# Optimization experiments

Hardware: AMD Instinct MI355X
Metric: run time of the kernel (lower is better)

## Reference

```python
import jax, jax.numpy as jnp
import numpy as np

B, S, D = 1, 2048, 4096          # batch, seqlen, model dim
H, KVH, HD = 32, 8, 128          # query heads, kv heads, head dim
W = 1024                         # sliding window
ROPE_THETA = 10000.0


def _rope(t, cos, sin):
    # t: [b, s, h, hd]; complex pairing matches torch.view_as_complex on reshape(..., hd//2, 2)
    a = t[..., 0::2]
    b = t[..., 1::2]
    out_r = a * cos - b * sin
    out_i = a * sin + b * cos
    return jnp.stack([out_r, out_i], axis=-1).reshape(t.shape)


def setup_inputs() -> dict:
    key = jax.random.key(0)
    ks = jax.random.split(key, 5)
    x = jax.random.normal(ks[0], (1, B, S, D), dtype=jnp.float32)
    wq = jax.random.normal(ks[1], (H * HD, D), dtype=jnp.float32) * 0.02
    wk = jax.random.normal(ks[2], (KVH * HD, D), dtype=jnp.float32) * 0.02
    wv = jax.random.normal(ks[3], (KVH * HD, D), dtype=jnp.float32) * 0.02
    wo = jax.random.normal(ks[4], (D, H * HD), dtype=jnp.float32) * 0.02
    # rotary frequencies: freqs_cis[s, hd/2] = exp(i * s * theta^{-2k/hd})
    inv_freq = 1.0 / (ROPE_THETA ** (jnp.arange(0, HD, 2, dtype=jnp.float32) / HD))
    angles = jnp.arange(S, dtype=jnp.float32)[:, None] * inv_freq[None, :]  # [S, HD/2]
    freqs_cos = jnp.cos(angles)
    freqs_sin = jnp.sin(angles)
    # sliding-window causal mask (additive)
    i = jnp.arange(S)
    allowed = (i[:, None] >= i[None, :]) & (i[:, None] - i[None, :] < W)
    mask = jnp.where(allowed, 0.0, -1e9).astype(jnp.float32)
    positions = jnp.arange(S, dtype=jnp.int64)
    return {"x": x, "wq": wq, "wk": wk, "wv": wv, "wo": wo,
            "freqs_cos": freqs_cos, "freqs_sin": freqs_sin,
            "mask": mask, "positions": positions}


def reference(x, wq, wk, wv, wo, freqs_cos, freqs_sin, mask, positions):
    xs = x[0]                                   # [B, S, D]
    xq = (xs @ wq.T).reshape(B, S, H, HD)
    xk = (xs @ wk.T).reshape(B, S, KVH, HD)
    xv = (xs @ wv.T).reshape(B, S, KVH, HD)
    cos = freqs_cos[None, :, None, :]           # [1, S, 1, HD/2]
    sin = freqs_sin[None, :, None, :]
    xq = _rope(xq, cos, sin)
    xk = _rope(xk, cos, sin)
    # GQA: repeat_interleave kv heads to match query heads (prefill path)
    rep = H // KVH
    k = jnp.repeat(xk, rep, axis=2)             # [B, S, H, HD]
    v = jnp.repeat(xv, rep, axis=2)
    scale = HD ** -0.5
    scores = jnp.einsum('bqhd,bkhd->bhqk', xq, k) * scale + mask[None, None]
    probs = jax.nn.softmax(scores, axis=-1)
    out = jnp.einsum('bhqk,bkhd->bqhd', probs, v).reshape(B, S, H * HD)
    return (out @ wo.T)[None]                   # [1, B, S, D]
```

## Files before the change

### kernel.cpp

```cpp
#include <hip/hip_runtime.h>
#include <hip/hip_bf16.h>


typedef __attribute__((ext_vector_type(8))) short short8;
typedef __attribute__((ext_vector_type(4))) float floatx4;
typedef unsigned short u16;
typedef unsigned int u32;

__device__ __forceinline__ u16 f2bf(float f) {
  u32 u = __builtin_bit_cast(u32, f);
  u32 r = u + 0x7FFFu + ((u >> 16) & 1u);
  return (u16)(r >> 16);
}

#define GLDS16(g, l)                                                     \
  __builtin_amdgcn_global_load_lds(                                      \
      (const __attribute__((address_space(1))) u32*)(g),                 \
      (__attribute__((address_space(3))) u32*)(l), 16, 0, 0)

#define SB() __builtin_amdgcn_sched_barrier(0)

__global__ __launch_bounds__(256) void cast_all(
    const float* __restrict__ x, const float* __restrict__ wq,
    const float* __restrict__ wk, const float* __restrict__ wv,
    const float* __restrict__ wo, u16* __restrict__ xb, u16* __restrict__ wqb,
    u16* __restrict__ wkb, u16* __restrict__ wvb, u16* __restrict__ wob) {
  const int tid = blockIdx.x * blockDim.x + threadIdx.x;
  const int stride = gridDim.x * blockDim.x;
  auto seg = [&](const float* __restrict__ in, u16* __restrict__ out, int n4) {
    for (int i = tid; i < n4; i += stride) {
      float4 v = ((const float4*)in)[i];
      ushort4 o;
      o.x = f2bf(v.x); o.y = f2bf(v.y); o.z = f2bf(v.z); o.w = f2bf(v.w);
      ((ushort4*)out)[i] = o;
    }
  };
  seg(x, xb, 2097152);
  seg(wq, wqb, 4194304);
  seg(wk, wkb, 1048576);
  seg(wv, wvb, 1048576);
  seg(wo, wob, 4194304);
}

template <int IS_QKV>
__global__ __launch_bounds__(512, 2) void gemm_t(
    const u16* __restrict__ A, const u16* __restrict__ B, void* __restrict__ Cq,
    u16* __restrict__ Ck, u16* __restrict__ Cv, const float* __restrict__ fcos,
    const float* __restrict__ fsin) {
  constexpr int BM = IS_QKV ? 256 : 128;
  constexpr int BN = IS_QKV ? 192 : 256;
  constexpr int MFR = BM / 32;
  constexpr int NFR = BN / 64;
  constexpr int WC = BN / 4;
  constexpr int ASZ = BM * 128;
  constexpr int BSZ = BN * 128;
  constexpr int NCA = ASZ / 8192;
  constexpr int NCB = BSZ / 8192;
  __shared__ u16 lds[(2 * ASZ + 3 * BSZ) / 2];
  const int K = 4096;

  int bm, bx;
  if constexpr (IS_QKV) {
    bm = blockIdx.x & 7;
    bx = blockIdx.x >> 3;
  } else {
    const int xcd = blockIdx.x & 7;
    const int j = blockIdx.x >> 3;
    bm = xcd * 2 + (j & 1);
    bx = j >> 1;
  }
  const int m0 = bm * BM, n0 = bx * BN;

  const int t = threadIdx.x, l = t & 63, w = t >> 6;
  const int li = l & 15, g = l >> 4;
  const int wm = w >> 2, wn = w & 3;

  const int srow = t >> 3;
  const int sslot = (t & 7) ^ (srow & 7);
  const u16* gA = A + (size_t)(m0 + srow) * K + sslot * 8;
  const u16* gB = B + (size_t)(n0 + srow) * K + sslot * 8;
  const int dst = t * 16;

  char* A0p = (char*)lds;
  char* A1p = A0p + ASZ;
  char* B0p = A0p + 2 * ASZ;
  char* B1p = B0p + BSZ;
  char* B2p = B1p + BSZ;

  auto stA = [&](char* base, int kt, int c) {
    GLDS16(gA + (size_t)c * 64 * K + kt, base + c * 8192 + dst);
  };
  auto stB = [&](char* base, int kt, int c) {
    GLDS16(gB + (size_t)c * 64 * K + kt, base + c * 8192 + dst);
  };

  int offA[2][MFR], offB[2][NFR];
#pragma unroll
  for (int kh = 0; kh < 2; kh++) {
#pragma unroll
    for (int mf = 0; mf < MFR; mf++) {
      int r = wm * (BM / 2) + mf * 16 + li;
      offA[kh][mf] = r * 128 + ((((kh << 2) | g) ^ (r & 7)) << 4);
    }
#pragma unroll
    for (int nf = 0; nf < NFR; nf++) {
      int r = wn * WC + nf * 16 + li;
      offB[kh][nf] = r * 128 + ((((kh << 2) | g) ^ (r & 7)) << 4);
    }
  }

  floatx4 acc[MFR][NFR] = {};
  const int NT = K / 64;

#pragma unroll
  for (int c = 0; c < NCB; c++) stB(B0p, 0, c);
#pragma unroll
  for (int c = 0; c < NCA; c++) stA(A0p, 0, c);
#pragma unroll
  for (int c = 0; c < NCB; c++) stB(B1p, 64, c);
  if constexpr (IS_QKV) asm volatile("s_waitcnt vmcnt(3)" ::: "memory");
  else                  asm volatile("s_waitcnt vmcnt(4)" ::: "memory");
  __builtin_amdgcn_s_barrier();

  for (int tt = 0; tt < NT; ++tt) {
    SB();
    const char* Ac = A0p;
    const char* Bc = B0p;
    const int kt1 = (tt + 1) * 64, kt2 = (tt + 2) * 64;
    const bool s1 = (tt + 1 < NT), s2 = (tt + 2 < NT);

    if constexpr (IS_QKV) {
      short8 a0[8], b0[3], a1[8], b1[3];
#pragma unroll
      for (int nf = 0; nf < 3; nf++) b0[nf] = *(const short8*)(Bc + offB[0][nf]);
#pragma unroll
      for (int mf = 0; mf < 8; mf++) a0[mf] = *(const short8*)(Ac + offA[0][mf]);
      if (s1) { stA(A1p, kt1, 0); stA(A1p, kt1, 1); stA(A1p, kt1, 2); stA(A1p, kt1, 3); }
#pragma unroll
      for (int mf = 0; mf < 8; mf++)
#pragma unroll
        for (int nf = 0; nf < 3; nf++)
          acc[mf][nf] = __builtin_amdgcn_mfma_f32_16x16x32_bf16(a0[mf], b0[nf], acc[mf][nf], 0, 0, 0);
#pragma unroll
      for (int nf = 0; nf < 3; nf++) b1[nf] = *(const short8*)(Bc + offB[1][nf]);
#pragma unroll
      for (int mf = 0; mf < 8; mf++) a1[mf] = *(const short8*)(Ac + offA[1][mf]);
      if (s2) { stB(B2p, kt2, 0); stB(B2p, kt2, 1); stB(B2p, kt2, 2); }
#pragma unroll
      for (int mf = 0; mf < 8; mf++)
#pragma unroll
        for (int nf = 0; nf < 3; nf++)
          acc[mf][nf] = __builtin_amdgcn_mfma_f32_16x16x32_bf16(a1[mf], b1[nf], acc[mf][nf], 0, 0, 0);
      SB();
      if (s2) asm volatile("s_waitcnt vmcnt(3)" ::: "memory");
      else    asm volatile("s_waitcnt vmcnt(0)" ::: "memory");
      __builtin_amdgcn_s_barrier();
    } else {
      short8 a0[4], b0[4], a1[4], b1[4];
#pragma unroll
      for (int mf = 0; mf < 4; mf++) a0[mf] = *(const short8*)(Ac + offA[0][mf]);
#pragma unroll
      for (int nf = 0; nf < 4; nf++) b0[nf] = *(const short8*)(Bc + offB[0][nf]);
      if (s1) { stA(A1p, kt1, 0); stA(A1p, kt1, 1); }
#pragma unroll
      for (int mf = 0; mf < 4; mf++)
#pragma unroll
        for (int nf = 0; nf < 4; nf++)
          acc[mf][nf] = __builtin_amdgcn_mfma_f32_16x16x32_bf16(a0[mf], b0[nf], acc[mf][nf], 0, 0, 0);
#pragma unroll
      for (int mf = 0; mf < 4; mf++) a1[mf] = *(const short8*)(Ac + offA[1][mf]);
#pragma unroll
      for (int nf = 0; nf < 4; nf++) b1[nf] = *(const short8*)(Bc + offB[1][nf]);
      if (s2) { stB(B2p, kt2, 0); stB(B2p, kt2, 1); stB(B2p, kt2, 2); stB(B2p, kt2, 3); }
#pragma unroll
      for (int mf = 0; mf < 4; mf++)
#pragma unroll
        for (int nf = 0; nf < 4; nf++)
          acc[mf][nf] = __builtin_amdgcn_mfma_f32_16x16x32_bf16(a1[mf], b1[nf], acc[mf][nf], 0, 0, 0);
      SB();
      if (s2) asm volatile("s_waitcnt vmcnt(4)" ::: "memory");
      else    asm volatile("s_waitcnt vmcnt(0)" ::: "memory");
      __builtin_amdgcn_s_barrier();
    }

    char* tmpA = A0p; A0p = A1p; A1p = tmpA;
    char* tmpB = B0p; B0p = B1p; B1p = B2p; B2p = tmpB;
  }

  const float scale = 0.08838834764831845f;
#pragma unroll
  for (int mf = 0; mf < MFR; mf++) {
#pragma unroll
    for (int nf = 0; nf < NFR; nf++) {
      const int row0 = m0 + wm * (BM / 2) + mf * 16 + 4 * g;
      const int c = n0 + wn * WC + nf * 16 + li;
      if constexpr (!IS_QKV) {
        float* Cf = (float*)Cq;
#pragma unroll
        for (int r = 0; r < 4; r++) Cf[(size_t)(row0 + r) * 4096 + c] = acc[mf][nf][r];
      } else {
        if (c < 5120) {
          const int hd = c & 127;
          const int pp = hd >> 1;
          const bool even = (hd & 1) == 0;
#pragma unroll
          for (int r = 0; r < 4; r++) {
            const int row = row0 + r;
            float cv = fcos[row * 64 + pp];
            float sv = fsin[row * 64 + pp];
            float v = acc[mf][nf][r];
            float pv = __shfl_xor(v, 1);
            float o = even ? (v * cv - pv * sv) : (pv * sv + v * cv);
            if (c < 4096) {
              ((u16*)Cq)[(size_t)row * 4096 + c] = f2bf(o * scale);
            } else {
              Ck[(size_t)row * 1024 + (c - 4096)] = f2bf(o);
            }
          }
        } else {
          u32 lo = (u32)f2bf(acc[mf][nf][0]) | ((u32)f2bf(acc[mf][nf][1]) << 16);
          u32 hi = (u32)f2bf(acc[mf][nf][2]) | ((u32)f2bf(acc[mf][nf][3]) << 16);
          uint2 val; val.x = lo; val.y = hi;
          *(uint2*)(&Cv[(size_t)(c - 5120) * 2048 + row0]) = val;
        }
      }
    }
  }
}

__global__ __launch_bounds__(256) void attn_kernel(const u16* __restrict__ Q,
                                                   const u16* __restrict__ K,
                                                   const u16* __restrict__ Vt,
                                                   u16* __restrict__ O) {
  __shared__ u16 Ks[2][64 * 128];
  __shared__ u16 Vs[2][128 * 64];
  __shared__ u16 Ps[4][16 * 72];

  const int t = threadIdx.x, l = t & 63, w = t >> 6;
  const int li = l & 15, g = l >> 4;
  const int q0 = blockIdx.x * 64;
  const int h = blockIdx.y;
  const int kvh = h >> 2;
  const int qw = q0 + w * 16;

  short8 qf[4];
  {
    const u16* qp = Q + (size_t)(qw + li) * 4096 + h * 128 + g * 8;
#pragma unroll
    for (int kk = 0; kk < 4; kk++) qf[kk] = *(const short8*)(qp + kk * 32);
  }

  const u16* gK[4];
  const u16* gV[4];
  int ldsOff[4];
#pragma unroll
  for (int i = 0; i < 4; i++) {
    int rK = 16 * w + 4 * i + (l >> 4);
    int sK = (l & 15) ^ (rK & 7);
    gK[i] = K + (size_t)rK * 1024 + kvh * 128 + sK * 8;
    int rV = 32 * w + 8 * i + (l >> 3);
    int sV = (l & 7) ^ (rV & 7);
    gV[i] = Vt + (size_t)(kvh * 128 + rV) * 2048 + sV * 8;
    ldsOff[i] = (4 * w + i) * 1024;
  }

  int offK[4][4];
#pragma unroll
  for (int n = 0; n < 4; n++) {
    int r = 16 * n + li;
#pragma unroll
    for (int kk = 0; kk < 4; kk++)
      offK[n][kk] = r * 256 + (((kk * 4 + g) ^ (r & 7)) << 4);
  }
  int offV[2][8];
#pragma unroll
  for (int kb = 0; kb < 2; kb++)
#pragma unroll
    for (int dt = 0; dt < 8; dt++) {
      int d = dt * 16 + li;
      offV[kb][dt] = d * 128 + (((kb * 4 + g) ^ (d & 7)) << 4);
    }

  float mrow[4] = {-1e30f, -1e30f, -1e30f, -1e30f};
  float lsum[4] = {0.f, 0.f, 0.f, 0.f};
  floatx4 accO[8] = {};

  int klo = q0 - 1023;
  if (klo < 0) klo = 0;
  klo &= ~63;
  const int nt = (q0 + 64 - klo) >> 6;

  auto stage = [&](int buf, int k0) {
    char* ksb = (char*)&Ks[buf][0];
    char* vsb = (char*)&Vs[buf][0];
#pragma unroll
    for (int i = 0; i < 4; i++) GLDS16(gK[i] + (size_t)k0 * 1024, ksb + ldsOff[i]);
#pragma unroll
    for (int i = 0; i < 4; i++) GLDS16(gV[i] + k0, vsb + ldsOff[i]);
  };

  stage(0, klo);
  asm volatile("s_waitcnt vmcnt(0)" ::: "memory");
  __builtin_amdgcn_s_barrier();

  for (int it = 0; it < nt; it++) {
    const int k0 = klo + (it << 6);
    if (it + 1 < nt) stage((it + 1) & 1, k0 + 64);

    if (k0 <= qw + 15 && k0 + 63 >= qw - 1023) {
      const char* kb = (const char*)&Ks[it & 1][0];
      const char* vb = (const char*)&Vs[it & 1][0];
      floatx4 s[4] = {};
      __builtin_amdgcn_s_setprio(1);
#pragma unroll
      for (int kk = 0; kk < 4; kk++)
#pragma unroll
        for (int n = 0; n < 4; n++) {
          short8 kf = *(const short8*)(kb + offK[n][kk]);
          s[n] = __builtin_amdgcn_mfma_f32_16x16x32_bf16(qf[kk], kf, s[n], 0, 0, 0);
        }
      __builtin_amdgcn_s_setprio(0);
      const bool full = (k0 + 63 <= qw) && (k0 >= qw + 15 - 1023);
      if (!full) {
#pragma unroll
        for (int n = 0; n < 4; n++) {
          const int kc = k0 + n * 16 + li;
#pragma unroll
          for (int r = 0; r < 4; r++) {
            const int qr = qw + 4 * g + r;
            if (kc > qr || qr - kc > 1023) s[n][r] = -__builtin_inff();
          }
        }
      }
      float rm[4];
#pragma unroll
      for (int r = 0; r < 4; r++)
        rm[r] = fmaxf(fmaxf(s[0][r], s[1][r]), fmaxf(s[2][r], s[3][r]));
#pragma unroll
      for (int msk = 1; msk <= 8; msk <<= 1)
#pragma unroll
        for (int r = 0; r < 4; r++) rm[r] = fmaxf(rm[r], __shfl_xor(rm[r], msk));
      float al[4];
#pragma unroll
      for (int r = 0; r < 4; r++) {
        float mn = fmaxf(mrow[r], rm[r]);
        al[r] = __expf(mrow[r] - mn);
        mrow[r] = mn;
        lsum[r] *= al[r];
      }
#pragma unroll
      for (int dt = 0; dt < 8; dt++)
#pragma unroll
        for (int r = 0; r < 4; r++) accO[dt][r] *= al[r];
      float rs[4] = {0.f, 0.f, 0.f, 0.f};
      u16* pw = &Ps[w][0];
#pragma unroll
      for (int n = 0; n < 4; n++)
#pragma unroll
        for (int r = 0; r < 4; r++) {
          float p = __expf(s[n][r] - mrow[r]);
          rs[r] += p;
          pw[(4 * g + r) * 72 + n * 16 + li] = f2bf(p);
        }
#pragma unroll
      for (int msk = 1; msk <= 8; msk <<= 1)
#pragma unroll
        for (int r = 0; r < 4; r++) rs[r] += __shfl_xor(rs[r], msk);
#pragma unroll
      for (int r = 0; r < 4; r++) lsum[r] += rs[r];
      short8 pa[2];
#pragma unroll
      for (int kbi = 0; kbi < 2; kbi++)
        pa[kbi] = *(const short8*)((const char*)&Ps[w][0] + li * 144 + kbi * 64 + g * 16);
      __builtin_amdgcn_s_setprio(1);
#pragma unroll
      for (int kbi = 0; kbi < 2; kbi++)
#pragma unroll
        for (int dt = 0; dt < 8; dt++) {
          short8 vf = *(const short8*)(vb + offV[kbi][dt]);
          accO[dt] = __builtin_amdgcn_mfma_f32_16x16x32_bf16(pa[kbi], vf, accO[dt], 0, 0, 0);
        }
      __builtin_amdgcn_s_setprio(0);
    }
    asm volatile("s_waitcnt vmcnt(0)" ::: "memory");
    __builtin_amdgcn_s_barrier();
  }

  float inv[4];
#pragma unroll
  for (int r = 0; r < 4; r++) inv[r] = 1.0f / lsum[r];
#pragma unroll
  for (int dt = 0; dt < 8; dt++)
#pragma unroll
    for (int r = 0; r < 4; r++)
      O[(size_t)(qw + 4 * g + r) * 4096 + h * 128 + dt * 16 + li] =
          f2bf(accO[dt][r] * inv[r]);
}

extern "C" void kernel_launch(void* const* d_in, const int* in_sizes, int n_in,
                              void* d_out, int out_size, void* d_ws, size_t ws_size,
                              hipStream_t stream) {
  const float* x    = (const float*)d_in[0];
  const float* wq   = (const float*)d_in[1];
  const float* wk   = (const float*)d_in[2];
  const float* wv   = (const float*)d_in[3];
  const float* wo   = (const float*)d_in[4];
  const float* fcos = (const float*)d_in[5];
  const float* fsin = (const float*)d_in[6];

  u16* ws  = (u16*)d_ws;
  u16* xb  = ws;
  u16* wqb = xb + 8388608;
  u16* wkb = wqb + 16777216;
  u16* wvb = wkb + 4194304;
  u16* wob = wvb + 4194304;
  u16* Qb  = wob + 16777216;
  u16* Kb  = Qb + 8388608;
  u16* Vtb = Kb + 2097152;
  u16* AOb = Vtb + 2097152;

  cast_all<<<2048, 256, 0, stream>>>(x, wq, wk, wv, wo, xb, wqb, wkb, wvb, wob);
  gemm_t<1><<<256, 512, 0, stream>>>(xb, wqb, Qb, Kb, Vtb, fcos, fsin);
  attn_kernel<<<dim3(32, 32), 256, 0, stream>>>(Qb, Kb, Vtb, AOb);
  gemm_t<0><<<256, 512, 0, stream>>>(AOb, wob, d_out, nullptr, nullptr, nullptr, nullptr);
}
```

Baseline: 314.7 us.

## Fuse fp32 weight bf16 conversion into GEMM B-tile loads via registers

Removes the standalone weight cast pass. The GEMMs now read fp32 weights directly through register-staged global loads, convert them to bf16, and write them to LDS, with B buffering reduced from three to two stages. This avoids writing and re-reading bf16 weight copies, but each GEMM block now fetches twice the bytes per weight tile (fp32) and repeats the conversion across M-blocks. It also adds register pressure and VALU work to the main loop.

```diff
diff --git a/kernel.cpp b/kernel.cpp
--- a/kernel.cpp
+++ b/kernel.cpp
@@ -18,35 +18,24 @@
       (const __attribute__((address_space(1))) u32*)(g),                 \
       (__attribute__((address_space(3))) u32*)(l), 16, 0, 0)
 
-#define SB() __builtin_amdgcn_sched_barrier(0)
-
-__global__ __launch_bounds__(256) void cast_all(
-    const float* __restrict__ x, const float* __restrict__ wq,
-    const float* __restrict__ wk, const float* __restrict__ wv,
-    const float* __restrict__ wo, u16* __restrict__ xb, u16* __restrict__ wqb,
-    u16* __restrict__ wkb, u16* __restrict__ wvb, u16* __restrict__ wob) {
-  const int tid = blockIdx.x * blockDim.x + threadIdx.x;
+__global__ __launch_bounds__(256) void cast_x(const float* __restrict__ in,
+                                              u16* __restrict__ out, int n4) {
+  int i = blockIdx.x * blockDim.x + threadIdx.x;
   const int stride = gridDim.x * blockDim.x;
-  auto seg = [&](const float* __restrict__ in, u16* __restrict__ out, int n4) {
-    for (int i = tid; i < n4; i += stride) {
-      float4 v = ((const float4*)in)[i];
-      ushort4 o;
-      o.x = f2bf(v.x); o.y = f2bf(v.y); o.z = f2bf(v.z); o.w = f2bf(v.w);
-      ((ushort4*)out)[i] = o;
-    }
-  };
-  seg(x, xb, 2097152);
-  seg(wq, wqb, 4194304);
-  seg(wk, wkb, 1048576);
-  seg(wv, wvb, 1048576);
-  seg(wo, wob, 4194304);
+  for (; i < n4; i += stride) {
+    float4 v = ((const float4*)in)[i];
+    ushort4 o;
+    o.x = f2bf(v.x); o.y = f2bf(v.y); o.z = f2bf(v.z); o.w = f2bf(v.w);
+    ((ushort4*)out)[i] = o;
+  }
 }
 
 template <int IS_QKV>
 __global__ __launch_bounds__(512, 2) void gemm_t(
-    const u16* __restrict__ A, const u16* __restrict__ B, void* __restrict__ Cq,
-    u16* __restrict__ Ck, u16* __restrict__ Cv, const float* __restrict__ fcos,
-    const float* __restrict__ fsin) {
+    const u16* __restrict__ A, const float* __restrict__ W0,
+    const float* __restrict__ W1, const float* __restrict__ W2,
+    void* __restrict__ Cq, u16* __restrict__ Ck, u16* __restrict__ Cv,
+    const float* __restrict__ fcos, const float* __restrict__ fsin) {
   constexpr int BM = IS_QKV ? 256 : 128;
   constexpr int BN = IS_QKV ? 192 : 256;
   constexpr int MFR = BM / 32;
@@ -56,7 +45,7 @@
   constexpr int BSZ = BN * 128;
   constexpr int NCA = ASZ / 8192;
   constexpr int NCB = BSZ / 8192;
-  __shared__ u16 lds[(2 * ASZ + 3 * BSZ) / 2];
+  __shared__ u16 lds[(2 * ASZ + 2 * BSZ) / 2];
   const int K = 4096;
 
   int bm, bx;
@@ -78,20 +67,52 @@
   const int srow = t >> 3;
   const int sslot = (t & 7) ^ (srow & 7);
   const u16* gA = A + (size_t)(m0 + srow) * K + sslot * 8;
-  const u16* gB = B + (size_t)(n0 + srow) * K + sslot * 8;
   const int dst = t * 16;
+
+  const float* gBc[NCB];
+#pragma unroll
+  for (int c = 0; c < NCB; c++) {
+    const int rowc = n0 + c * 64 + srow;
+    const float* src;
+    if constexpr (IS_QKV) {
+      src = (rowc < 4096)   ? W0 + (size_t)rowc * K
+          : (rowc < 5120)   ? W1 + (size_t)(rowc - 4096) * K
+                            : W2 + (size_t)(rowc - 5120) * K;
+    } else {
+      src = W0 + (size_t)rowc * K;
+    }
+    gBc[c] = src + sslot * 8;
+  }
 
   char* A0p = (char*)lds;
   char* A1p = A0p + ASZ;
   char* B0p = A0p + 2 * ASZ;
   char* B1p = B0p + BSZ;
-  char* B2p = B1p + BSZ;
-
-  auto stA = [&](char* base, int kt, int c) {
-    GLDS16(gA + (size_t)c * 64 * K + kt, base + c * 8192 + dst);
+
+  auto stA = [&](char* base, int kt) {
+#pragma unroll
+    for (int c = 0; c < NCA; c++)
+      GLDS16(gA + (size_t)c * 64 * K + kt, base + c * 8192 + dst);
   };
-  auto stB = [&](char* base, int kt, int c) {
-    GLDS16(gB + (size_t)c * 64 * K + kt, base + c * 8192 + dst);
+
+  float4 bv[NCB][2];
+  auto loadB = [&](int kt) {
+#pragma unroll
+    for (int c = 0; c < NCB; c++) {
+      bv[c][0] = *(const float4*)(gBc[c] + kt);
+      bv[c][1] = *(const float4*)(gBc[c] + kt + 4);
+    }
+  };
+  auto writeB = [&](char* base) {
+#pragma unroll
+    for (int c = 0; c < NCB; c++) {
+      u32 w0 = (u32)f2bf(bv[c][0].x) | ((u32)f2bf(bv[c][0].y) << 16);
+      u32 w1 = (u32)f2bf(bv[c][0].z) | ((u32)f2bf(bv[c][0].w) << 16);
+      u32 w2 = (u32)f2bf(bv[c][1].x) | ((u32)f2bf(bv[c][1].y) << 16);
+      u32 w3 = (u32)f2bf(bv[c][1].z) | ((u32)f2bf(bv[c][1].w) << 16);
+      uint4 pk; pk.x = w0; pk.y = w1; pk.z = w2; pk.w = w3;
+      *(uint4*)(base + c * 8192 + dst) = pk;
+    }
   };
 
   int offA[2][MFR], offB[2][NFR];
@@ -112,22 +133,25 @@
   floatx4 acc[MFR][NFR] = {};
   const int NT = K / 64;
 
-#pragma unroll
-  for (int c = 0; c < NCB; c++) stB(B0p, 0, c);
-#pragma unroll
-  for (int c = 0; c < NCA; c++) stA(A0p, 0, c);
-#pragma unroll
-  for (int c = 0; c < NCB; c++) stB(B1p, 64, c);
-  if constexpr (IS_QKV) asm volatile("s_waitcnt vmcnt(3)" ::: "memory");
-  else                  asm volatile("s_waitcnt vmcnt(4)" ::: "memory");
+  loadB(0);
+  stA(A0p, 0);
+  writeB(B0p);
+  loadB(64);
+  if constexpr (IS_QKV) asm volatile("s_waitcnt vmcnt(6)" ::: "memory");
+  else                  asm volatile("s_waitcnt vmcnt(8)" ::: "memory");
+  asm volatile("s_waitcnt lgkmcnt(0)" ::: "memory");
   __builtin_amdgcn_s_barrier();
 
   for (int tt = 0; tt < NT; ++tt) {
-    SB();
-    const char* Ac = A0p;
-    const char* Bc = B0p;
-    const int kt1 = (tt + 1) * 64, kt2 = (tt + 2) * 64;
+    const char* Ac = (tt & 1) ? A1p : A0p;
+    const char* Bc = (tt & 1) ? B1p : B0p;
+    char* Aw = (tt & 1) ? A0p : A1p;
+    char* Bw = (tt & 1) ? B0p : B1p;
     const bool s1 = (tt + 1 < NT), s2 = (tt + 2 < NT);
+
+    if (s1) writeB(Bw);
+    if (s1) stA(Aw, (tt + 1) * 64);
+    if (s2) loadB((tt + 2) * 64);
 
     if constexpr (IS_QKV) {
       short8 a0[8], b0[3], a1[8], b1[3];
@@ -135,7 +159,6 @@
       for (int nf = 0; nf < 3; nf++) b0[nf] = *(const short8*)(Bc + offB[0][nf]);
 #pragma unroll
       for (int mf = 0; mf < 8; mf++) a0[mf] = *(const short8*)(Ac + offA[0][mf]);
-      if (s1) { stA(A1p, kt1, 0); stA(A1p, kt1, 1); stA(A1p, kt1, 2); stA(A1p, kt1, 3); }
 #pragma unroll
       for (int mf = 0; mf < 8; mf++)
 #pragma unroll
@@ -145,23 +168,17 @@
       for (int nf = 0; nf < 3; nf++) b1[nf] = *(const short8*)(Bc + offB[1][nf]);
 #pragma unroll
       for (int mf = 0; mf < 8; mf++) a1[mf] = *(const short8*)(Ac + offA[1][mf]);
-      if (s2) { stB(B2p, kt2, 0); stB(B2p, kt2, 1); stB(B2p, kt2, 2); }
 #pragma unroll
       for (int mf = 0; mf < 8; mf++)
 #pragma unroll
         for (int nf = 0; nf < 3; nf++)
           acc[mf][nf] = __builtin_amdgcn_mfma_f32_16x16x32_bf16(a1[mf], b1[nf], acc[mf][nf], 0, 0, 0);
-      SB();
-      if (s2) asm volatile("s_waitcnt vmcnt(3)" ::: "memory");
-      else    asm volatile("s_waitcnt vmcnt(0)" ::: "memory");
-      __builtin_amdgcn_s_barrier();
     } else {
       short8 a0[4], b0[4], a1[4], b1[4];
 #pragma unroll
       for (int mf = 0; mf < 4; mf++) a0[mf] = *(const short8*)(Ac + offA[0][mf]);
 #pragma unroll
       for (int nf = 0; nf < 4; nf++) b0[nf] = *(const short8*)(Bc + offB[0][nf]);
-      if (s1) { stA(A1p, kt1, 0); stA(A1p, kt1, 1); }
 #pragma unroll
       for (int mf = 0; mf < 4; mf++)
 #pragma unroll
@@ -171,20 +188,21 @@
       for (int mf = 0; mf < 4; mf++) a1[mf] = *(const short8*)(Ac + offA[1][mf]);
 #pragma unroll
       for (int nf = 0; nf < 4; nf++) b1[nf] = *(const short8*)(Bc + offB[1][nf]);
-      if (s2) { stB(B2p, kt2, 0); stB(B2p, kt2, 1); stB(B2p, kt2, 2); stB(B2p, kt2, 3); }
 #pragma unroll
       for (int mf = 0; mf < 4; mf++)
 #pragma unroll
         for (int nf = 0; nf < 4; nf++)
           acc[mf][nf] = __builtin_amdgcn_mfma_f32_16x16x32_bf16(a1[mf], b1[nf], acc[mf][nf], 0, 0, 0);
-      SB();
-      if (s2) asm volatile("s_waitcnt vmcnt(4)" ::: "memory");
-      else    asm volatile("s_waitcnt vmcnt(0)" ::: "memory");
-      __builtin_amdgcn_s_barrier();
-    }
-
-    char* tmpA = A0p; A0p = A1p; A1p = tmpA;
-    char* tmpB = B0p; B0p = B1p; B1p = B2p; B2p = tmpB;
+    }
+
+    asm volatile("s_waitcnt lgkmcnt(0)" ::: "memory");
+    if (s2) {
+      if constexpr (IS_QKV) asm volatile("s_waitcnt vmcnt(6)" ::: "memory");
+      else                  asm volatile("s_waitcnt vmcnt(8)" ::: "memory");
+    } else if (s1) {
+      asm volatile("s_waitcnt vmcnt(0)" ::: "memory");
+    }
+    __builtin_amdgcn_s_barrier();
   }
 
   const float scale = 0.08838834764831845f;
@@ -410,17 +428,13 @@
 
   u16* ws  = (u16*)d_ws;
   u16* xb  = ws;
-  u16* wqb = xb + 8388608;
-  u16* wkb = wqb + 16777216;
-  u16* wvb = wkb + 4194304;
-  u16* wob = wvb + 4194304;
-  u16* Qb  = wob + 16777216;
+  u16* Qb  = xb + 8388608;
   u16* Kb  = Qb + 8388608;
   u16* Vtb = Kb + 2097152;
   u16* AOb = Vtb + 2097152;
 
-  cast_all<<<2048, 256, 0, stream>>>(x, wq, wk, wv, wo, xb, wqb, wkb, wvb, wob);
-  gemm_t<1><<<256, 512, 0, stream>>>(xb, wqb, Qb, Kb, Vtb, fcos, fsin);
+  cast_x<<<2048, 256, 0, stream>>>(x, xb, 2097152);
+  gemm_t<1><<<256, 512, 0, stream>>>(xb, wq, wk, wv, Qb, Kb, Vtb, fcos, fsin);
   attn_kernel<<<dim3(32, 32), 256, 0, stream>>>(Qb, Kb, Vtb, AOb);
-  gemm_t<0><<<256, 512, 0, stream>>>(AOb, wob, d_out, nullptr, nullptr, nullptr, nullptr);
+  gemm_t<0><<<256, 512, 0, stream>>>(AOb, wo, nullptr, nullptr, d_out, nullptr, nullptr, nullptr, nullptr);
 }
```

Result: slower. 341.3 us (+8.5%).

## Fuse x cast into QKV GEMM loads and wo cast into attention kernel

Applied to the files above, without the earlier changes.

The QKV GEMM now reads fp32 x directly through register loads, converts to bf16 and writes to LDS, which removes the separate x cast pass and its bf16 round trip through memory. The wo fp32-to-bf16 cast is moved into the prologue of the attention kernel so it runs there instead of in the standalone cast kernel. The standalone cast kernel now only handles wq/wk/wv. In exchange the GEMM A path loses async global_load_lds, uses more registers and ALU work for conversion, and doubles A-side global bytes. The attention kernel also gains extra memory traffic at its start.

```diff
diff --git a/kernel.cpp b/kernel.cpp
--- a/kernel.cpp
+++ b/kernel.cpp
@@ -20,11 +20,10 @@
 
 #define SB() __builtin_amdgcn_sched_barrier(0)
 
-__global__ __launch_bounds__(256) void cast_all(
-    const float* __restrict__ x, const float* __restrict__ wq,
-    const float* __restrict__ wk, const float* __restrict__ wv,
-    const float* __restrict__ wo, u16* __restrict__ xb, u16* __restrict__ wqb,
-    u16* __restrict__ wkb, u16* __restrict__ wvb, u16* __restrict__ wob) {
+__global__ __launch_bounds__(256) void cast_w(
+    const float* __restrict__ wq, const float* __restrict__ wk,
+    const float* __restrict__ wv, u16* __restrict__ wqb,
+    u16* __restrict__ wkb, u16* __restrict__ wvb) {
   const int tid = blockIdx.x * blockDim.x + threadIdx.x;
   const int stride = gridDim.x * blockDim.x;
   auto seg = [&](const float* __restrict__ in, u16* __restrict__ out, int n4) {
@@ -35,18 +34,16 @@
       ((ushort4*)out)[i] = o;
     }
   };
-  seg(x, xb, 2097152);
   seg(wq, wqb, 4194304);
   seg(wk, wkb, 1048576);
   seg(wv, wvb, 1048576);
-  seg(wo, wob, 4194304);
 }
 
 template <int IS_QKV>
 __global__ __launch_bounds__(512, 2) void gemm_t(
-    const u16* __restrict__ A, const u16* __restrict__ B, void* __restrict__ Cq,
-    u16* __restrict__ Ck, u16* __restrict__ Cv, const float* __restrict__ fcos,
-    const float* __restrict__ fsin) {
+    const void* __restrict__ Araw, const u16* __restrict__ B,
+    void* __restrict__ Cq, u16* __restrict__ Ck, u16* __restrict__ Cv,
+    const float* __restrict__ fcos, const float* __restrict__ fsin) {
   constexpr int BM = IS_QKV ? 256 : 128;
   constexpr int BN = IS_QKV ? 192 : 256;
   constexpr int MFR = BM / 32;
@@ -77,9 +74,11 @@
 
   const int srow = t >> 3;
   const int sslot = (t & 7) ^ (srow & 7);
-  const u16* gA = A + (size_t)(m0 + srow) * K + sslot * 8;
   const u16* gB = B + (size_t)(n0 + srow) * K + sslot * 8;
   const int dst = t * 16;
+
+  const float* gAf = (const float*)Araw + (size_t)(m0 + srow) * K + sslot * 8;
+  const u16* gA = (const u16*)Araw + (size_t)(m0 + srow) * K + sslot * 8;
 
   char* A0p = (char*)lds;
   char* A1p = A0p + ASZ;
@@ -94,6 +93,27 @@
     GLDS16(gB + (size_t)c * 64 * K + kt, base + c * 8192 + dst);
   };
 
+  float4 av[NCA][2];
+  auto loadA = [&](int kt) {
+#pragma unroll
+    for (int c = 0; c < NCA; c++) {
+      const float* p = gAf + (size_t)c * 64 * K + kt;
+      av[c][0] = *(const float4*)(p);
+      av[c][1] = *(const float4*)(p + 4);
+    }
+  };
+  auto writeA = [&](char* base) {
+#pragma unroll
+    for (int c = 0; c < NCA; c++) {
+      u32 w0 = (u32)f2bf(av[c][0].x) | ((u32)f2bf(av[c][0].y) << 16);
+      u32 w1 = (u32)f2bf(av[c][0].z) | ((u32)f2bf(av[c][0].w) << 16);
+      u32 w2 = (u32)f2bf(av[c][1].x) | ((u32)f2bf(av[c][1].y) << 16);
+      u32 w3 = (u32)f2bf(av[c][1].z) | ((u32)f2bf(av[c][1].w) << 16);
+      uint4 pk; pk.x = w0; pk.y = w1; pk.z = w2; pk.w = w3;
+      *(uint4*)(base + c * 8192 + dst) = pk;
+    }
+  };
+
   int offA[2][MFR], offB[2][NFR];
 #pragma unroll
   for (int kh = 0; kh < 2; kh++) {
@@ -112,30 +132,43 @@
   floatx4 acc[MFR][NFR] = {};
   const int NT = K / 64;
 
-#pragma unroll
-  for (int c = 0; c < NCB; c++) stB(B0p, 0, c);
-#pragma unroll
-  for (int c = 0; c < NCA; c++) stA(A0p, 0, c);
-#pragma unroll
-  for (int c = 0; c < NCB; c++) stB(B1p, 64, c);
-  if constexpr (IS_QKV) asm volatile("s_waitcnt vmcnt(3)" ::: "memory");
-  else                  asm volatile("s_waitcnt vmcnt(4)" ::: "memory");
-  __builtin_amdgcn_s_barrier();
+  if constexpr (IS_QKV) {
+#pragma unroll
+    for (int c = 0; c < NCB; c++) stB(B0p, 0, c);
+    loadA(0);
+    writeA(A0p);
+#pragma unroll
+    for (int c = 0; c < NCB; c++) stB(B1p, 64, c);
+    loadA(64);
+    asm volatile("s_waitcnt lgkmcnt(0)" ::: "memory");
+    __builtin_amdgcn_s_barrier();
+  } else {
+#pragma unroll
+    for (int c = 0; c < NCB; c++) stB(B0p, 0, c);
+#pragma unroll
+    for (int c = 0; c < NCA; c++) stA(A0p, 0, c);
+#pragma unroll
+    for (int c = 0; c < NCB; c++) stB(B1p, 64, c);
+    asm volatile("s_waitcnt vmcnt(4)" ::: "memory");
+    __builtin_amdgcn_s_barrier();
+  }
 
   for (int tt = 0; tt < NT; ++tt) {
     SB();
-    const char* Ac = A0p;
-    const char* Bc = B0p;
     const int kt1 = (tt + 1) * 64, kt2 = (tt + 2) * 64;
     const bool s1 = (tt + 1 < NT), s2 = (tt + 2 < NT);
 
     if constexpr (IS_QKV) {
+      const char* Ac = (tt & 1) ? A1p : A0p;
+      char* Aw = (tt & 1) ? A0p : A1p;
+      const char* Bc = B0p;
+      if (s1) writeA(Aw);
       short8 a0[8], b0[3], a1[8], b1[3];
 #pragma unroll
       for (int nf = 0; nf < 3; nf++) b0[nf] = *(const short8*)(Bc + offB[0][nf]);
 #pragma unroll
       for (int mf = 0; mf < 8; mf++) a0[mf] = *(const short8*)(Ac + offA[0][mf]);
-      if (s1) { stA(A1p, kt1, 0); stA(A1p, kt1, 1); stA(A1p, kt1, 2); stA(A1p, kt1, 3); }
+      if (s2) { stB(B2p, kt2, 0); stB(B2p, kt2, 1); stB(B2p, kt2, 2); }
 #pragma unroll
       for (int mf = 0; mf < 8; mf++)
 #pragma unroll
@@ -145,17 +178,18 @@
       for (int nf = 0; nf < 3; nf++) b1[nf] = *(const short8*)(Bc + offB[1][nf]);
 #pragma unroll
       for (int mf = 0; mf < 8; mf++) a1[mf] = *(const short8*)(Ac + offA[1][mf]);
-      if (s2) { stB(B2p, kt2, 0); stB(B2p, kt2, 1); stB(B2p, kt2, 2); }
+      if (s2) loadA(kt2);
 #pragma unroll
       for (int mf = 0; mf < 8; mf++)
 #pragma unroll
         for (int nf = 0; nf < 3; nf++)
           acc[mf][nf] = __builtin_amdgcn_mfma_f32_16x16x32_bf16(a1[mf], b1[nf], acc[mf][nf], 0, 0, 0);
       SB();
-      if (s2) asm volatile("s_waitcnt vmcnt(3)" ::: "memory");
-      else    asm volatile("s_waitcnt vmcnt(0)" ::: "memory");
+      asm volatile("s_waitcnt lgkmcnt(0)" ::: "memory");
       __builtin_amdgcn_s_barrier();
     } else {
+      const char* Ac = A0p;
+      const char* Bc = B0p;
       short8 a0[4], b0[4], a1[4], b1[4];
 #pragma unroll
       for (int mf = 0; mf < 4; mf++) a0[mf] = *(const short8*)(Ac + offA[0][mf]);
@@ -181,9 +215,9 @@
       if (s2) asm volatile("s_waitcnt vmcnt(4)" ::: "memory");
       else    asm volatile("s_waitcnt vmcnt(0)" ::: "memory");
       __builtin_amdgcn_s_barrier();
-    }
-
-    char* tmpA = A0p; A0p = A1p; A1p = tmpA;
+      char* tmpA = A0p; A0p = A1p; A1p = tmpA;
+    }
+
     char* tmpB = B0p; B0p = B1p; B1p = B2p; B2p = tmpB;
   }
 
@@ -231,10 +265,24 @@
 __global__ __launch_bounds__(256) void attn_kernel(const u16* __restrict__ Q,
                                                    const u16* __restrict__ K,
                                                    const u16* __restrict__ Vt,
-                                                   u16* __restrict__ O) {
+                                                   u16* __restrict__ O,
+                                                   const float* __restrict__ wo,
+                                                   u16* __restrict__ wob) {
   __shared__ u16 Ks[2][64 * 128];
   __shared__ u16 Vs[2][128 * 64];
   __shared__ u16 Ps[4][16 * 72];
+
+  {
+    const int gid = (blockIdx.y * gridDim.x + blockIdx.x) * 256 + threadIdx.x;
+#pragma unroll 4
+    for (int i = 0; i < 16; i++) {
+      const size_t idx = (size_t)gid + (size_t)i * 262144;
+      float4 v = ((const float4*)wo)[idx];
+      ushort4 o;
+      o.x = f2bf(v.x); o.y = f2bf(v.y); o.z = f2bf(v.z); o.w = f2bf(v.w);
+      ((ushort4*)wob)[idx] = o;
+    }
+  }
 
   const int t = threadIdx.x, l = t & 63, w = t >> 6;
   const int li = l & 15, g = l >> 4;
@@ -409,8 +457,7 @@
   const float* fsin = (const float*)d_in[6];
 
   u16* ws  = (u16*)d_ws;
-  u16* xb  = ws;
-  u16* wqb = xb + 8388608;
+  u16* wqb = ws;
   u16* wkb = wqb + 16777216;
   u16* wvb = wkb + 4194304;
   u16* wob = wvb + 4194304;
@@ -419,8 +466,8 @@
   u16* Vtb = Kb + 2097152;
   u16* AOb = Vtb + 2097152;
 
-  cast_all<<<2048, 256, 0, stream>>>(x, wq, wk, wv, wo, xb, wqb, wkb, wvb, wob);
-  gemm_t<1><<<256, 512, 0, stream>>>(xb, wqb, Qb, Kb, Vtb, fcos, fsin);
-  attn_kernel<<<dim3(32, 32), 256, 0, stream>>>(Qb, Kb, Vtb, AOb);
+  cast_w<<<1024, 256, 0, stream>>>(wq, wk, wv, wqb, wkb, wvb);
+  gemm_t<1><<<256, 512, 0, stream>>>(x, wqb, Qb, Kb, Vtb, fcos, fsin);
+  attn_kernel<<<dim3(32, 32), 256, 0, stream>>>(Qb, Kb, Vtb, AOb, wo, wob);
   gemm_t<0><<<256, 512, 0, stream>>>(AOb, wob, d_out, nullptr, nullptr, nullptr, nullptr);
 }
```

Result: slower. 405.2 us (+28.7%).
